# Performance work log

Measured on AMD Instinct MI355X. Metric: run time of the kernel, lower is better.

The kernel has to match this reference:

```python
import jax, jax.numpy as jnp
import numpy as np

B, S, D, H = 2, 2048, 2048, 16
HD = D // H  # head_dim = 128


def setup_inputs() -> dict:
    key = jax.random.key(0)
    ks = jax.random.split(key, 9)
    std = 0.02
    x = jax.random.normal(ks[0], (B, S, D), dtype=jnp.float32)
    Wq = jax.random.normal(ks[1], (D, D), dtype=jnp.float32) * std
    bq = jnp.zeros((D,), dtype=jnp.float32)
    Wk = jax.random.normal(ks[2], (D, D), dtype=jnp.float32) * std
    bk = jnp.zeros((D,), dtype=jnp.float32)
    Wv = jax.random.normal(ks[3], (D, D), dtype=jnp.float32) * std
    bv = jnp.zeros((D,), dtype=jnp.float32)
    Wo = jax.random.normal(ks[4], (D, D), dtype=jnp.float32) * std
    bo = jnp.zeros((D,), dtype=jnp.float32)
    return {"x": x, "Wq": Wq, "bq": bq, "Wk": Wk, "bk": bk,
            "Wv": Wv, "bv": bv, "Wo": Wo, "bo": bo}


def _rope_tables(seq_len, head_dim, base=10000.0):
    # inv_freq over even indices; freqs: [S, HD/2]
    inv_freq = 1.0 / (base ** (jnp.arange(0, head_dim, 2, dtype=jnp.float32) / head_dim))
    t = jnp.arange(seq_len, dtype=jnp.float32)
    freqs = jnp.einsum('i,j->ij', t, inv_freq)
    return jnp.cos(freqs), jnp.sin(freqs)  # each [S, HD/2]


def _rotate(x, cos, sin):
    # x: [B, H, S, HD]; cos/sin: [S, HD/2] broadcast over B,H
    x1, x2 = jnp.split(x, 2, axis=-1)
    return jnp.concatenate([x1 * cos - x2 * sin, x1 * sin + x2 * cos], axis=-1)


def reference(x, Wq, bq, Wk, bk, Wv, bv, Wo, bo):
    b, s, d = x.shape
    q = (jnp.einsum('bsd,df->bsf', x, Wq) + bq).reshape(b, s, H, HD).transpose(0, 2, 1, 3)
    k = (jnp.einsum('bsd,df->bsf', x, Wk) + bk).reshape(b, s, H, HD).transpose(0, 2, 1, 3)
    v = (jnp.einsum('bsd,df->bsf', x, Wv) + bv).reshape(b, s, H, HD).transpose(0, 2, 1, 3)
    cos, sin = _rope_tables(s, HD)
    qr = _rotate(q, cos, sin)
    kr = _rotate(k, cos, sin)
    scores = jnp.einsum('bhqd,bhkd->bhqk', qr, kr) / jnp.sqrt(jnp.float32(HD))
    probs = jax.nn.softmax(scores, axis=-1)
    out = jnp.einsum('bhqk,bhkd->bhqd', probs, v)
    out = out.transpose(0, 2, 1, 3).reshape(b, s, d)
    return jnp.einsum('bsd,df->bsf', out, Wo) + bo
```

## Files before the change

kernel.cpp:

```cpp
#include <hip/hip_runtime.h>

#define BB  2
#define SS  2048
#define DD  2048
#define HH  16
#define HDD 128
#define BSR 4096

using short8  = __attribute__((ext_vector_type(8))) short;
using floatx4 = __attribute__((ext_vector_type(4))) float;

__device__ __forceinline__ float bf2f(unsigned short u) {
  return __uint_as_float(((unsigned int)u) << 16);
}
__device__ __forceinline__ unsigned short f2bf(float f) {
  unsigned int u = __float_as_uint(f);
  u += 0x7fffu + ((u >> 16) & 1u);
  return (unsigned short)(u >> 16);
}
__device__ __forceinline__ unsigned int pk2bf(float a, float b) {
  unsigned int ua = __float_as_uint(a);
  ua += 0x7fffu + ((ua >> 16) & 1u);
  unsigned int ub = __float_as_uint(b);
  ub += 0x7fffu + ((ub >> 16) & 1u);
  return (ua >> 16) | (ub & 0xffff0000u);
}
__device__ __forceinline__ float fexp2(float x) {
#if __has_builtin(__builtin_amdgcn_exp2f)
  return __builtin_amdgcn_exp2f(x);
#else
  return __expf(x * 0.6931471805599453f);
#endif
}
__device__ __forceinline__ void gl_lds16(const void* g, void* l) {
  __builtin_amdgcn_global_load_lds(
      (__attribute__((address_space(1))) void*)g,
      (__attribute__((address_space(3))) void*)l, 16, 0, 0);
}

__global__ __launch_bounds__(256) void transpose_w(
    const float* __restrict__ Wq, const float* __restrict__ Wk,
    const float* __restrict__ Wv, const float* __restrict__ Wo,
    unsigned short* __restrict__ wqkvt, unsigned short* __restrict__ wot)
{
  __shared__ float tile[32][33];
  const float* W; unsigned short* Out;
  int z = blockIdx.z;
  if      (z == 0) { W = Wq; Out = wqkvt; }
  else if (z == 1) { W = Wk; Out = wqkvt + (size_t)DD * DD; }
  else if (z == 2) { W = Wv; Out = wqkvt + 2 * (size_t)DD * DD; }
  else             { W = Wo; Out = wot; }
  int tx = threadIdx.x, ty = threadIdx.y;
  int d0 = blockIdx.y * 32, f0 = blockIdx.x * 32;
#pragma unroll
  for (int i = 0; i < 4; i++)
    tile[ty + i * 8][tx] = W[(size_t)(d0 + ty + i * 8) * DD + f0 + tx];
  __syncthreads();
#pragma unroll
  for (int i = 0; i < 4; i++)
    Out[(size_t)(f0 + ty + i * 8) * DD + d0 + tx] = f2bf(tile[tx][ty + i * 8]);
}

__global__ __launch_bounds__(256) void conv_x(const float* __restrict__ x,
                                              unsigned short* __restrict__ xb)
{
  size_t i = ((size_t)blockIdx.x * 256 + threadIdx.x) * 4;
  float4 v = *(const float4*)(x + i);
  ushort4 o;
  o.x = f2bf(v.x); o.y = f2bf(v.y); o.z = f2bf(v.z); o.w = f2bf(v.w);
  *(ushort4*)(xb + i) = o;
}

__global__ __launch_bounds__(256) void rope_tab(float2* __restrict__ rtab) {
  int idx = blockIdx.x * 256 + threadIdx.x;
  int s = idx >> 6, c = idx & 63;
  float inv = powf(10000.f, -(float)c * (1.f / 64.f));
  float ang = (float)s * inv;
  float sn, cc;
  sincosf(ang, &sn, &cc);
  rtab[idx] = make_float2(cc, sn);
}

#define MFMA_QUAD(MB, NB, FB) \
  _Pragma("unroll") for (int m_ = 0; m_ < 4; m_++) \
  _Pragma("unroll") for (int n_ = 0; n_ < 2; n_++) \
  _Pragma("unroll") for (int kk_ = 0; kk_ < 2; kk_++) \
    acc[(MB)+m_][(NB)+n_] = __builtin_amdgcn_mfma_f32_16x16x32_bf16( \
        fa[m_][kk_], FB[n_][kk_], acc[(MB)+m_][(NB)+n_], 0, 0, 0);
#define BARX __builtin_amdgcn_s_barrier()

__global__ __launch_bounds__(512) void gemm_qkv(
    const unsigned short* __restrict__ A, const unsigned short* __restrict__ Bt,
    const float* __restrict__ bq, const float* __restrict__ bk,
    const float* __restrict__ bv, const float2* __restrict__ rtab,
    unsigned short* __restrict__ q_r, unsigned short* __restrict__ k_r,
    unsigned short* __restrict__ v_t)
{
  __shared__ unsigned short smem[65536];
  unsigned short* const AsP[2] = { smem,         smem + 32768 };
  unsigned short* const BsP[2] = { smem + 16384, smem + 49152 };
  const int K = DD;
  int t = threadIdx.x;
  int lane = t & 63, qd = lane >> 4, l16 = lane & 15;
  int w = t >> 6, wr = w >> 2, wc = w & 3;

  int bid = blockIdx.y * gridDim.x + blockIdx.x;
  int wg  = (bid & 7) * 48 + (bid >> 3);
  int n0 = (wg % 24) * 256;
  int m0 = (wg / 24) * 256;

  floatx4 zero4 = {0.f, 0.f, 0.f, 0.f};
  floatx4 acc[8][4];
#pragma unroll
  for (int i = 0; i < 8; i++)
#pragma unroll
    for (int j = 0; j < 4; j++) acc[i][j] = zero4;

  int srow = t >> 3;
  int schunk = ((t & 7) ^ (srow & 7)) * 8;
  const unsigned short* Ag = A  + (size_t)(m0 + srow) * K + schunk;
  const unsigned short* Bg = Bt + (size_t)(n0 + srow) * K + schunk;

  auto stA = [&](int bf, int kt, int half) {
#pragma unroll
    for (int q = 0; q < 2; q++) {
      int c = half * 2 + q;
      gl_lds16(Ag + (size_t)c * 64 * K + kt * 64, AsP[bf] + ((size_t)c * 512 + t) * 8);
    }
  };
  auto stB = [&](int bf, int kt, int half) {
#pragma unroll
    for (int q = 0; q < 2; q++) {
      int c = half * 2 + q;
      gl_lds16(Bg + (size_t)c * 64 * K + kt * 64, BsP[bf] + ((size_t)c * 512 + t) * 8);
    }
  };
  auto ldA = [&](int bf, int mf, int kk) -> short8 {
    int row = wr * 128 + mf * 16 + l16;
    return *(const short8*)&AsP[bf][row * 64 + (((kk * 4 + qd) ^ (l16 & 7)) * 8)];
  };
  auto ldB = [&](int bf, int nf, int kk) -> short8 {
    int row = wc * 64 + nf * 16 + l16;
    return *(const short8*)&BsP[bf][row * 64 + (((kk * 4 + qd) ^ (l16 & 7)) * 8)];
  };

  stA(0, 0, 0); stA(0, 0, 1); stB(0, 0, 0); stB(0, 0, 1);
  stA(1, 1, 0);
  asm volatile("s_waitcnt vmcnt(2)" ::: "memory");
  BARX;

  short8 fa[4][2], fbl[2][2], fbh[2][2];

#pragma unroll 1
  for (int i = 0; i < 16; i++) {
    const bool full = (i < 15);
    const int kt1 = 2 * i + 1, kt2 = 2 * i + 2, kt3 = 2 * i + 3;

#pragma unroll
    for (int m = 0; m < 4; m++) { fa[m][0] = ldA(0, m, 0); fa[m][1] = ldA(0, m, 1); }
#pragma unroll
    for (int n = 0; n < 2; n++) { fbl[n][0] = ldB(0, n, 0); fbl[n][1] = ldB(0, n, 1); }
    stA(1, kt1, 1);
    BARX;
    __builtin_amdgcn_s_setprio(1);
    MFMA_QUAD(0, 0, fbl);
    __builtin_amdgcn_s_setprio(0);
    BARX;
#pragma unroll
    for (int n = 0; n < 2; n++) { fbh[n][0] = ldB(0, 2 + n, 0); fbh[n][1] = ldB(0, 2 + n, 1); }
    stB(1, kt1, 0);
    BARX;
    __builtin_amdgcn_s_setprio(1);
    MFMA_QUAD(0, 2, fbh);
    __builtin_amdgcn_s_setprio(0);
    BARX;
#pragma unroll
    for (int m = 0; m < 4; m++) { fa[m][0] = ldA(0, 4 + m, 0); fa[m][1] = ldA(0, 4 + m, 1); }
    stB(1, kt1, 1);
    BARX;
    __builtin_amdgcn_s_setprio(1);
    MFMA_QUAD(4, 0, fbl);
    __builtin_amdgcn_s_setprio(0);
    BARX;
    if (full) stA(0, kt2, 0);
    BARX;
    __builtin_amdgcn_s_setprio(1);
    MFMA_QUAD(4, 2, fbh);
    __builtin_amdgcn_s_setprio(0);
    if (full) asm volatile("s_waitcnt vmcnt(2)" ::: "memory");
    else      asm volatile("s_waitcnt vmcnt(0)" ::: "memory");
    BARX;

#pragma unroll
    for (int m = 0; m < 4; m++) { fa[m][0] = ldA(1, m, 0); fa[m][1] = ldA(1, m, 1); }
#pragma unroll
    for (int n = 0; n < 2; n++) { fbl[n][0] = ldB(1, n, 0); fbl[n][1] = ldB(1, n, 1); }
    if (full) stA(0, kt2, 1);
    BARX;
    __builtin_amdgcn_s_setprio(1);
    MFMA_QUAD(0, 0, fbl);
    __builtin_amdgcn_s_setprio(0);
    BARX;
#pragma unroll
    for (int n = 0; n < 2; n++) { fbh[n][0] = ldB(1, 2 + n, 0); fbh[n][1] = ldB(1, 2 + n, 1); }
    if (full) stB(0, kt2, 0);
    BARX;
    __builtin_amdgcn_s_setprio(1);
    MFMA_QUAD(0, 2, fbh);
    __builtin_amdgcn_s_setprio(0);
    BARX;
#pragma unroll
    for (int m = 0; m < 4; m++) { fa[m][0] = ldA(1, 4 + m, 0); fa[m][1] = ldA(1, 4 + m, 1); }
    if (full) stB(0, kt2, 1);
    BARX;
    __builtin_amdgcn_s_setprio(1);
    MFMA_QUAD(4, 0, fbl);
    __builtin_amdgcn_s_setprio(0);
    BARX;
    if (full) stA(1, kt3, 0);
    BARX;
    __builtin_amdgcn_s_setprio(1);
    MFMA_QUAD(4, 2, fbh);
    __builtin_amdgcn_s_setprio(0);
    if (full) asm volatile("s_waitcnt vmcnt(2)" ::: "memory");
    else      asm volatile("s_waitcnt vmcnt(0)" ::: "memory");
    BARX;
  }

  __syncthreads();
  int plane = n0 >> 11;
  int h0 = (n0 >> 7) & 15;
  const float* bias = plane == 0 ? bq : (plane == 1 ? bk : bv);
  int bI = m0 >> 11, sbase = m0 & (SS - 1);
  const int CT = 258;
  unsigned short* Ct = smem;

#pragma unroll 1
  for (int half = 0; half < 2; half++) {
    if (wr == half) {
#pragma unroll
      for (int mf = 0; mf < 8; mf++)
#pragma unroll
        for (int nf = 0; nf < 4; nf++) {
          int rl = mf * 16 + qd * 4;
          int cl = wc * 64 + nf * 16 + l16;
          float bsv = bias[h0 * 128 + cl];
#pragma unroll
          for (int r = 0; r < 4; r++)
            Ct[(rl + r) * CT + cl] = f2bf(acc[mf][nf][r] + bsv);
        }
    }
    __syncthreads();
    if (plane < 2) {
      unsigned short* dst0 = (plane == 0 ? q_r : k_r) + (size_t)(bI * HH + h0) * SS * HDD;
      const float fac = (plane == 0) ? 0.12751744f : 1.0f;
#pragma unroll
      for (int it = 0; it < 16; it++) {
        int idx = it * 512 + t;
        int rl = idx >> 6;
        int u = idx & 63; int hh = u >> 5; int c2 = (u & 31) * 2;
        int s = sbase + half * 128 + rl;
        float4 cs = *(const float4*)&rtab[(size_t)s * 64 + c2];
        int cb = hh * 128 + c2;
        float a0 = bf2f(Ct[rl * CT + cb]);
        float a1 = bf2f(Ct[rl * CT + cb + 1]);
        float b0 = bf2f(Ct[rl * CT + cb + 64]);
        float b1 = bf2f(Ct[rl * CT + cb + 65]);
        unsigned int lo = pk2bf((a0 * cs.x - b0 * cs.y) * fac,
                                (a1 * cs.z - b1 * cs.w) * fac);
        unsigned int hi = pk2bf((a0 * cs.y + b0 * cs.x) * fac,
                                (a1 * cs.w + b1 * cs.z) * fac);
        unsigned short* dst = dst0 + (size_t)hh * SS * HDD;
        size_t rowb = (size_t)s * HDD;
        *(unsigned int*)&dst[rowb + c2]      = lo;
        *(unsigned int*)&dst[rowb + c2 + 64] = hi;
      }
    } else {
      unsigned short* dst0 = v_t + (size_t)(bI * HH + h0) * HDD * SS;
#pragma unroll
      for (int it = 0; it < 32; it++) {
        int idx = it * 512 + t;
        int hdg = idx >> 6;
        int sp = (idx & 63) * 2;
        unsigned short v0 = Ct[sp * CT + hdg];
        unsigned short v1 = Ct[(sp + 1) * CT + hdg];
        int hh = hdg >> 7, hd = hdg & 127;
        int y = sp & 63;
        int kap = ((y >> 5) & 1) * 32 + ((y >> 2) & 3) * 8 + ((y >> 4) & 1) * 4 + (y & 3);
        int sg = sbase + half * 128 + (sp & ~63) + kap;
        unsigned short* dst = dst0 + (size_t)hh * HDD * SS;
        *(unsigned int*)&dst[(size_t)hd * SS + sg] = ((unsigned int)v1 << 16) | v0;
      }
    }
    if (half == 0) __syncthreads();
  }
}

template <bool OUTF32>
__global__ __launch_bounds__(256) void gemm_bt(
    const unsigned short* __restrict__ A, const unsigned short* __restrict__ Bt,
    const float* __restrict__ bias, void* __restrict__ Cout,
    int M, int N, int K)
{
  __shared__ unsigned short As[128 * 64];
  __shared__ unsigned short Bs[128 * 64];
  int t = threadIdx.x;
  int m0 = blockIdx.y * 128, n0 = blockIdx.x * 128;
  int w = t >> 6, lane = t & 63, qd = lane >> 4, l16 = lane & 15;
  int wm = (w >> 1) * 64, wn = (w & 1) * 64;
  floatx4 zero4 = {0.f, 0.f, 0.f, 0.f};
  floatx4 acc[4][4];
#pragma unroll
  for (int i = 0; i < 4; i++)
#pragma unroll
    for (int j = 0; j < 4; j++) acc[i][j] = zero4;

  int gchunk = (t & 7) ^ ((t >> 3) & 7);
  const unsigned short* Ab = A  + (size_t)(m0 + (t >> 3)) * K + gchunk * 8;
  const unsigned short* Bb = Bt + (size_t)(n0 + (t >> 3)) * K + gchunk * 8;
  size_t qK = (size_t)32 * K;

  for (int k0 = 0; k0 < K; k0 += 64) {
    __syncthreads();
#pragma unroll
    for (int c = 0; c < 4; c++) {
      gl_lds16(Ab + c * qK + k0, &As[(c * 256 + t) * 8]);
      gl_lds16(Bb + c * qK + k0, &Bs[(c * 256 + t) * 8]);
    }
    __syncthreads();
#pragma unroll
    for (int ks = 0; ks < 2; ks++) {
      int ch = ((ks * 4 + qd) ^ (l16 & 7)) * 8;
      short8 af[4], bfr[4];
#pragma unroll
      for (int i = 0; i < 4; i++)
        af[i] = *(const short8*)&As[(wm + i * 16 + l16) * 64 + ch];
#pragma unroll
      for (int j = 0; j < 4; j++)
        bfr[j] = *(const short8*)&Bs[(wn + j * 16 + l16) * 64 + ch];
#pragma unroll
      for (int i = 0; i < 4; i++)
#pragma unroll
        for (int j = 0; j < 4; j++)
          acc[i][j] = __builtin_amdgcn_mfma_f32_16x16x32_bf16(af[i], bfr[j], acc[i][j], 0, 0, 0);
    }
  }

#pragma unroll
  for (int i = 0; i < 4; i++)
#pragma unroll
    for (int j = 0; j < 4; j++) {
      int row = m0 + wm + i * 16 + qd * 4;
      int col = n0 + wn + j * 16 + l16;
      float bsv = bias ? bias[col] : 0.f;
#pragma unroll
      for (int r = 0; r < 4; r++) {
        float v = acc[i][j][r] + bsv;
        if (OUTF32) ((float*)Cout)[(size_t)(row + r) * N + col] = v;
        else ((unsigned short*)Cout)[(size_t)(row + r) * N + col] = f2bf(v);
      }
    }
}

__global__ __launch_bounds__(256, 2) void attn_kernel(
    const unsigned short* __restrict__ q_r, const unsigned short* __restrict__ k_r,
    const unsigned short* __restrict__ v_t, unsigned short* __restrict__ aout)
{
  __shared__ unsigned short Ks[2][64 * 128];
  __shared__ unsigned short Vs[2][128 * 64];
  int t = threadIdx.x, w = t >> 6, lane = t & 63, qd = lane >> 4, l16 = lane & 15;
  int L = blockIdx.y * gridDim.x + blockIdx.x;
  int jj = L >> 3;
  int bh = (L & 7) * 4 + (jj >> 4);
  int q0 = (jj & 15) * 128;
  const unsigned short* qb = q_r + (size_t)bh * SS * HDD;
  const unsigned short* kb = k_r + (size_t)bh * SS * HDD;
  const unsigned short* vb = v_t + (size_t)bh * HDD * SS;

  short8 aq[2][4];
#pragma unroll
  for (int mi = 0; mi < 2; mi++)
#pragma unroll
    for (int ks = 0; ks < 4; ks++)
      aq[mi][ks] = *(const short8*)
          &qb[(size_t)(q0 + w * 32 + mi * 16 + l16) * HDD + ks * 32 + qd * 8];

  float m_i[2], l_i[2];
  floatx4 zero4 = {0.f, 0.f, 0.f, 0.f};
  floatx4 o[2][8];
#pragma unroll
  for (int mi = 0; mi < 2; mi++) { m_i[mi] = -1e30f; l_i[mi] = 0.f; }
#pragma unroll
  for (int mi = 0; mi < 2; mi++)
#pragma unroll
    for (int n = 0; n < 8; n++) o[mi][n] = zero4;

  auto stage = [&](int nb, int kt) {
#pragma unroll
    for (int c = 0; c < 4; c++) {
      int flat = c * 256 + t;
      int r = flat >> 4, cc = flat & 15;
      gl_lds16(kb + (size_t)(kt + r) * HDD + (cc ^ (r & 15)) * 8, &Ks[nb][flat * 8]);
    }
#pragma unroll
    for (int c = 0; c < 4; c++) {
      int flat = c * 256 + t;
      int r = flat >> 3, cc = flat & 7;
      gl_lds16(vb + (size_t)r * SS + kt + (cc ^ (r & 7)) * 8, &Vs[nb][flat * 8]);
    }
  };

  stage(0, 0);
  int buf = 0;

  for (int kt = 0; kt < SS; kt += 64) {
    __syncthreads();
    if (kt + 64 < SS) stage(buf ^ 1, kt + 64);

    floatx4 sc[2][4];
#pragma unroll
    for (int mi = 0; mi < 2; mi++)
#pragma unroll
      for (int j = 0; j < 4; j++) sc[mi][j] = zero4;
#pragma unroll
    for (int j = 0; j < 4; j++) {
      int krow = j * 16 + l16;
#pragma unroll
      for (int ks = 0; ks < 4; ks++) {
        int chunk = ks * 4 + qd;
        short8 kf = *(const short8*)&Ks[buf][krow * 128 + ((chunk ^ (krow & 15)) * 8)];
        sc[0][j] = __builtin_amdgcn_mfma_f32_16x16x32_bf16(kf, aq[0][ks], sc[0][j], 0, 0, 0);
        sc[1][j] = __builtin_amdgcn_mfma_f32_16x16x32_bf16(kf, aq[1][ks], sc[1][j], 0, 0, 0);
      }
    }

    float rmax[2];
#pragma unroll
    for (int mi = 0; mi < 2; mi++) {
      float m = sc[mi][0][0];
#pragma unroll
      for (int j = 0; j < 4; j++)
#pragma unroll
        for (int r = 0; r < 4; r++) m = fmaxf(m, sc[mi][j][r]);
      m = fmaxf(m, __shfl_xor(m, 16, 64));
      m = fmaxf(m, __shfl_xor(m, 32, 64));
      rmax[mi] = m;
    }

    bool up = (rmax[0] > m_i[0]) || (rmax[1] > m_i[1]);
    if (__ballot(up) != 0ull) {
#pragma unroll
      for (int mi = 0; mi < 2; mi++) {
        float mn = fmaxf(m_i[mi], rmax[mi]);
        float a = fexp2(m_i[mi] - mn);
        m_i[mi] = mn;
        l_i[mi] *= a;
#pragma unroll
        for (int n = 0; n < 8; n++)
#pragma unroll
          for (int r = 0; r < 4; r++) o[mi][n][r] *= a;
      }
    }

    unsigned int pr[2][4][2];
#pragma unroll
    for (int mi = 0; mi < 2; mi++) {
      float s0 = 0.f;
#pragma unroll
      for (int j = 0; j < 4; j++) {
        float p0 = fexp2(sc[mi][j][0] - m_i[mi]);
        float p1 = fexp2(sc[mi][j][1] - m_i[mi]);
        float p2 = fexp2(sc[mi][j][2] - m_i[mi]);
        float p3 = fexp2(sc[mi][j][3] - m_i[mi]);
        s0 += (p0 + p1) + (p2 + p3);
        pr[mi][j][0] = pk2bf(p0, p1);
        pr[mi][j][1] = pk2bf(p2, p3);
      }
      s0 += __shfl_xor(s0, 16, 64);
      s0 += __shfl_xor(s0, 32, 64);
      l_i[mi] += s0;
    }

#pragma unroll
    for (int n = 0; n < 8; n++) {
      int vrow = n * 16 + l16;
#pragma unroll
      for (int ks = 0; ks < 2; ks++) {
        int chunk = ks * 4 + qd;
        short8 av = *(const short8*)&Vs[buf][vrow * 64 + ((chunk ^ (vrow & 7)) * 8)];
        union { unsigned int u[4]; short8 v; } bp0, bp1;
        bp0.u[0] = pr[0][2 * ks][0];     bp0.u[1] = pr[0][2 * ks][1];
        bp0.u[2] = pr[0][2 * ks + 1][0]; bp0.u[3] = pr[0][2 * ks + 1][1];
        bp1.u[0] = pr[1][2 * ks][0];     bp1.u[1] = pr[1][2 * ks][1];
        bp1.u[2] = pr[1][2 * ks + 1][0]; bp1.u[3] = pr[1][2 * ks + 1][1];
        o[0][n] = __builtin_amdgcn_mfma_f32_16x16x32_bf16(av, bp0.v, o[0][n], 0, 0, 0);
        o[1][n] = __builtin_amdgcn_mfma_f32_16x16x32_bf16(av, bp1.v, o[1][n], 0, 0, 0);
      }
    }
    buf ^= 1;
  }

  int b = bh >> 4, h = bh & 15;
#pragma unroll
  for (int mi = 0; mi < 2; mi++) {
    int qrow = q0 + w * 32 + mi * 16 + l16;
    float inv_l = 1.f / l_i[mi];
    size_t base = ((size_t)(b * SS + qrow)) * DD + h * HDD;
#pragma unroll
    for (int n = 0; n < 8; n++) {
      uint2 pkd;
      pkd.x = pk2bf(o[mi][n][0] * inv_l, o[mi][n][1] * inv_l);
      pkd.y = pk2bf(o[mi][n][2] * inv_l, o[mi][n][3] * inv_l);
      *(uint2*)&aout[base + n * 16 + qd * 4] = pkd;
    }
  }
}

extern "C" void kernel_launch(void* const* d_in, const int* in_sizes, int n_in,
                              void* d_out, int out_size, void* d_ws, size_t ws_size,
                              hipStream_t stream) {
  const float* x  = (const float*)d_in[0];
  const float* Wq = (const float*)d_in[1];
  const float* bq = (const float*)d_in[2];
  const float* Wk = (const float*)d_in[3];
  const float* bk = (const float*)d_in[4];
  const float* Wv = (const float*)d_in[5];
  const float* bv = (const float*)d_in[6];
  const float* Wo = (const float*)d_in[7];
  const float* bo = (const float*)d_in[8];
  float* out = (float*)d_out;

  char* ws = (char*)d_ws;
  unsigned short* xb      = (unsigned short*)(ws + 0);
  unsigned short* wqkvt   = (unsigned short*)(ws + 16777216);
  unsigned short* wot     = (unsigned short*)(ws + 41943040);
  float2*         rtab    = (float2*)(ws + 50331648);
  unsigned short* q_r     = (unsigned short*)(ws + 100663296);
  unsigned short* k_r     = (unsigned short*)(ws + 117440512);
  unsigned short* v_t     = (unsigned short*)(ws + 134217728);
  unsigned short* attn_o  = xb;

  transpose_w<<<dim3(DD / 32, DD / 32, 4), dim3(32, 8), 0, stream>>>(
      Wq, Wk, Wv, Wo, wqkvt, wot);
  conv_x<<<dim3((BSR * DD) / 1024), dim3(256), 0, stream>>>(x, xb);
  rope_tab<<<dim3((SS * 64) / 256), dim3(256), 0, stream>>>(rtab);
  gemm_qkv<<<dim3(3 * DD / 256, BSR / 256), dim3(512), 0, stream>>>(
      xb, wqkvt, bq, bk, bv, rtab, q_r, k_r, v_t);
  attn_kernel<<<dim3(SS / 128, BB * HH), dim3(256), 0, stream>>>(
      q_r, k_r, v_t, attn_o);
  gemm_bt<true><<<dim3(DD / 128, BSR / 128), dim3(256), 0, stream>>>(
      attn_o, wot, bo, out, BSR, DD, DD);
}
```

Baseline: 411.7 us.

## Shrink QKV GEMM tile to 128x256 and rework k-loop pipeline

The fused QKV GEMM block tile shrinks from 256x256 to 128x256, which doubles the grid to 768 blocks and halves the accumulator registers and A-tile LDS. The k-loop is rewritten as a KTILE macro that prefetches the tile two steps ahead into the same buffer, with vmcnt(6) waits. The aim is more blocks for the 256 CUs and higher occupancy from fewer registers and less LDS. The cost is lower arithmetic intensity per block, so B (weight) tiles are reloaded twice as often. The epilogue becomes a single pass because the 128-row tile fits the transpose buffer.

```diff
diff --git a/kernel.cpp b/kernel.cpp
--- a/kernel.cpp
+++ b/kernel.cpp
@@ -81,13 +81,37 @@
   rtab[idx] = make_float2(cc, sn);
 }
 
-#define MFMA_QUAD(MB, NB, FB) \
-  _Pragma("unroll") for (int m_ = 0; m_ < 4; m_++) \
+#define MFMA_Q(MB, NB, FA, FB) \
+  _Pragma("unroll") for (int m_ = 0; m_ < 2; m_++) \
   _Pragma("unroll") for (int n_ = 0; n_ < 2; n_++) \
   _Pragma("unroll") for (int kk_ = 0; kk_ < 2; kk_++) \
     acc[(MB)+m_][(NB)+n_] = __builtin_amdgcn_mfma_f32_16x16x32_bf16( \
-        fa[m_][kk_], FB[n_][kk_], acc[(MB)+m_][(NB)+n_], 0, 0, 0);
+        (FA)[m_][kk_], (FB)[n_][kk_], acc[(MB)+m_][(NB)+n_], 0, 0, 0);
 #define BARX __builtin_amdgcn_s_barrier()
+
+#define KTILE(BF, KT, FULL) do {                                               \
+  _Pragma("unroll")                                                            \
+  for (int m = 0; m < 2; m++) { fa[m][0] = ldA(BF, m, 0); fa[m][1] = ldA(BF, m, 1); } \
+  _Pragma("unroll")                                                            \
+  for (int n = 0; n < 2; n++) { fbl[n][0] = ldB(BF, n, 0); fbl[n][1] = ldB(BF, n, 1); } \
+  BARX; __builtin_amdgcn_s_setprio(1); MFMA_Q(0, 0, fa, fbl);                  \
+  __builtin_amdgcn_s_setprio(0); BARX;                                         \
+  _Pragma("unroll")                                                            \
+  for (int n = 0; n < 2; n++) { fbh[n][0] = ldB(BF, 2 + n, 0); fbh[n][1] = ldB(BF, 2 + n, 1); } \
+  BARX; __builtin_amdgcn_s_setprio(1); MFMA_Q(0, 2, fa, fbh);                  \
+  __builtin_amdgcn_s_setprio(0); BARX;                                         \
+  _Pragma("unroll")                                                            \
+  for (int m = 0; m < 2; m++) { fa2[m][0] = ldA(BF, 2 + m, 0); fa2[m][1] = ldA(BF, 2 + m, 1); } \
+  if (FULL) stB(BF, (KT) + 2, 0);                                              \
+  BARX; __builtin_amdgcn_s_setprio(1); MFMA_Q(2, 0, fa2, fbl);                 \
+  __builtin_amdgcn_s_setprio(0); BARX;                                         \
+  if (FULL) { stB(BF, (KT) + 2, 1); stA(BF, (KT) + 2); }                       \
+  BARX; __builtin_amdgcn_s_setprio(1); MFMA_Q(2, 2, fa2, fbh);                 \
+  __builtin_amdgcn_s_setprio(0);                                               \
+  if (FULL) asm volatile("s_waitcnt vmcnt(6)" ::: "memory");                   \
+  else      asm volatile("s_waitcnt vmcnt(0)" ::: "memory");                   \
+  BARX;                                                                        \
+} while (0)
 
 __global__ __launch_bounds__(512) void gemm_qkv(
     const unsigned short* __restrict__ A, const unsigned short* __restrict__ Bt,
@@ -96,23 +120,23 @@
     unsigned short* __restrict__ q_r, unsigned short* __restrict__ k_r,
     unsigned short* __restrict__ v_t)
 {
-  __shared__ unsigned short smem[65536];
-  unsigned short* const AsP[2] = { smem,         smem + 32768 };
-  unsigned short* const BsP[2] = { smem + 16384, smem + 49152 };
+  __shared__ unsigned short smem[49152];
+  unsigned short* const AsP[2] = { smem,          smem + 24576 };
+  unsigned short* const BsP[2] = { smem + 8192,   smem + 32768 };
   const int K = DD;
   int t = threadIdx.x;
   int lane = t & 63, qd = lane >> 4, l16 = lane & 15;
   int w = t >> 6, wr = w >> 2, wc = w & 3;
 
-  int bid = blockIdx.y * gridDim.x + blockIdx.x;
-  int wg  = (bid & 7) * 48 + (bid >> 3);
-  int n0 = (wg % 24) * 256;
-  int m0 = (wg / 24) * 256;
+  int bid = blockIdx.x;
+  int wg  = (bid & 7) * 96 + (bid >> 3);
+  int n0 = (wg / 32) * 256;
+  int m0 = (wg % 32) * 128;
 
   floatx4 zero4 = {0.f, 0.f, 0.f, 0.f};
-  floatx4 acc[8][4];
-#pragma unroll
-  for (int i = 0; i < 8; i++)
+  floatx4 acc[4][4];
+#pragma unroll
+  for (int i = 0; i < 4; i++)
 #pragma unroll
     for (int j = 0; j < 4; j++) acc[i][j] = zero4;
 
@@ -121,12 +145,10 @@
   const unsigned short* Ag = A  + (size_t)(m0 + srow) * K + schunk;
   const unsigned short* Bg = Bt + (size_t)(n0 + srow) * K + schunk;
 
-  auto stA = [&](int bf, int kt, int half) {
-#pragma unroll
-    for (int q = 0; q < 2; q++) {
-      int c = half * 2 + q;
+  auto stA = [&](int bf, int kt) {
+#pragma unroll
+    for (int c = 0; c < 2; c++)
       gl_lds16(Ag + (size_t)c * 64 * K + kt * 64, AsP[bf] + ((size_t)c * 512 + t) * 8);
-    }
   };
   auto stB = [&](int bf, int kt, int half) {
 #pragma unroll
@@ -136,7 +158,7 @@
     }
   };
   auto ldA = [&](int bf, int mf, int kk) -> short8 {
-    int row = wr * 128 + mf * 16 + l16;
+    int row = wr * 64 + mf * 16 + l16;
     return *(const short8*)&AsP[bf][row * 64 + (((kk * 4 + qd) ^ (l16 & 7)) * 8)];
   };
   auto ldB = [&](int bf, int nf, int kk) -> short8 {
@@ -144,87 +166,18 @@
     return *(const short8*)&BsP[bf][row * 64 + (((kk * 4 + qd) ^ (l16 & 7)) * 8)];
   };
 
-  stA(0, 0, 0); stA(0, 0, 1); stB(0, 0, 0); stB(0, 0, 1);
-  stA(1, 1, 0);
-  asm volatile("s_waitcnt vmcnt(2)" ::: "memory");
+  stA(0, 0); stB(0, 0, 0); stB(0, 0, 1);
+  stA(1, 1); stB(1, 1, 0); stB(1, 1, 1);
+  asm volatile("s_waitcnt vmcnt(6)" ::: "memory");
   BARX;
 
-  short8 fa[4][2], fbl[2][2], fbh[2][2];
+  short8 fa[2][2], fa2[2][2], fbl[2][2], fbh[2][2];
 
 #pragma unroll 1
   for (int i = 0; i < 16; i++) {
     const bool full = (i < 15);
-    const int kt1 = 2 * i + 1, kt2 = 2 * i + 2, kt3 = 2 * i + 3;
-
-#pragma unroll
-    for (int m = 0; m < 4; m++) { fa[m][0] = ldA(0, m, 0); fa[m][1] = ldA(0, m, 1); }
-#pragma unroll
-    for (int n = 0; n < 2; n++) { fbl[n][0] = ldB(0, n, 0); fbl[n][1] = ldB(0, n, 1); }
-    stA(1, kt1, 1);
-    BARX;
-    __builtin_amdgcn_s_setprio(1);
-    MFMA_QUAD(0, 0, fbl);
-    __builtin_amdgcn_s_setprio(0);
-    BARX;
-#pragma unroll
-    for (int n = 0; n < 2; n++) { fbh[n][0] = ldB(0, 2 + n, 0); fbh[n][1] = ldB(0, 2 + n, 1); }
-    stB(1, kt1, 0);
-    BARX;
-    __builtin_amdgcn_s_setprio(1);
-    MFMA_QUAD(0, 2, fbh);
-    __builtin_amdgcn_s_setprio(0);
-    BARX;
-#pragma unroll
-    for (int m = 0; m < 4; m++) { fa[m][0] = ldA(0, 4 + m, 0); fa[m][1] = ldA(0, 4 + m, 1); }
-    stB(1, kt1, 1);
-    BARX;
-    __builtin_amdgcn_s_setprio(1);
-    MFMA_QUAD(4, 0, fbl);
-    __builtin_amdgcn_s_setprio(0);
-    BARX;
-    if (full) stA(0, kt2, 0);
-    BARX;
-    __builtin_amdgcn_s_setprio(1);
-    MFMA_QUAD(4, 2, fbh);
-    __builtin_amdgcn_s_setprio(0);
-    if (full) asm volatile("s_waitcnt vmcnt(2)" ::: "memory");
-    else      asm volatile("s_waitcnt vmcnt(0)" ::: "memory");
-    BARX;
-
-#pragma unroll
-    for (int m = 0; m < 4; m++) { fa[m][0] = ldA(1, m, 0); fa[m][1] = ldA(1, m, 1); }
-#pragma unroll
-    for (int n = 0; n < 2; n++) { fbl[n][0] = ldB(1, n, 0); fbl[n][1] = ldB(1, n, 1); }
-    if (full) stA(0, kt2, 1);
-    BARX;
-    __builtin_amdgcn_s_setprio(1);
-    MFMA_QUAD(0, 0, fbl);
-    __builtin_amdgcn_s_setprio(0);
-    BARX;
-#pragma unroll
-    for (int n = 0; n < 2; n++) { fbh[n][0] = ldB(1, 2 + n, 0); fbh[n][1] = ldB(1, 2 + n, 1); }
-    if (full) stB(0, kt2, 0);
-    BARX;
-    __builtin_amdgcn_s_setprio(1);
-    MFMA_QUAD(0, 2, fbh);
-    __builtin_amdgcn_s_setprio(0);
-    BARX;
-#pragma unroll
-    for (int m = 0; m < 4; m++) { fa[m][0] = ldA(1, 4 + m, 0); fa[m][1] = ldA(1, 4 + m, 1); }
-    if (full) stB(0, kt2, 1);
-    BARX;
-    __builtin_amdgcn_s_setprio(1);
-    MFMA_QUAD(4, 0, fbl);
-    __builtin_amdgcn_s_setprio(0);
-    BARX;
-    if (full) stA(1, kt3, 0);
-    BARX;
-    __builtin_amdgcn_s_setprio(1);
-    MFMA_QUAD(4, 2, fbh);
-    __builtin_amdgcn_s_setprio(0);
-    if (full) asm volatile("s_waitcnt vmcnt(2)" ::: "memory");
-    else      asm volatile("s_waitcnt vmcnt(0)" ::: "memory");
-    BARX;
+    KTILE(0, 2 * i,     full);
+    KTILE(1, 2 * i + 1, full);
   }
 
   __syncthreads();
@@ -235,64 +188,59 @@
   const int CT = 258;
   unsigned short* Ct = smem;
 
-#pragma unroll 1
-  for (int half = 0; half < 2; half++) {
-    if (wr == half) {
-#pragma unroll
-      for (int mf = 0; mf < 8; mf++)
-#pragma unroll
-        for (int nf = 0; nf < 4; nf++) {
-          int rl = mf * 16 + qd * 4;
-          int cl = wc * 64 + nf * 16 + l16;
-          float bsv = bias[h0 * 128 + cl];
-#pragma unroll
-          for (int r = 0; r < 4; r++)
-            Ct[(rl + r) * CT + cl] = f2bf(acc[mf][nf][r] + bsv);
-        }
-    }
-    __syncthreads();
-    if (plane < 2) {
-      unsigned short* dst0 = (plane == 0 ? q_r : k_r) + (size_t)(bI * HH + h0) * SS * HDD;
-      const float fac = (plane == 0) ? 0.12751744f : 1.0f;
-#pragma unroll
-      for (int it = 0; it < 16; it++) {
-        int idx = it * 512 + t;
-        int rl = idx >> 6;
-        int u = idx & 63; int hh = u >> 5; int c2 = (u & 31) * 2;
-        int s = sbase + half * 128 + rl;
-        float4 cs = *(const float4*)&rtab[(size_t)s * 64 + c2];
-        int cb = hh * 128 + c2;
-        float a0 = bf2f(Ct[rl * CT + cb]);
-        float a1 = bf2f(Ct[rl * CT + cb + 1]);
-        float b0 = bf2f(Ct[rl * CT + cb + 64]);
-        float b1 = bf2f(Ct[rl * CT + cb + 65]);
-        unsigned int lo = pk2bf((a0 * cs.x - b0 * cs.y) * fac,
-                                (a1 * cs.z - b1 * cs.w) * fac);
-        unsigned int hi = pk2bf((a0 * cs.y + b0 * cs.x) * fac,
-                                (a1 * cs.w + b1 * cs.z) * fac);
-        unsigned short* dst = dst0 + (size_t)hh * SS * HDD;
-        size_t rowb = (size_t)s * HDD;
-        *(unsigned int*)&dst[rowb + c2]      = lo;
-        *(unsigned int*)&dst[rowb + c2 + 64] = hi;
-      }
-    } else {
-      unsigned short* dst0 = v_t + (size_t)(bI * HH + h0) * HDD * SS;
-#pragma unroll
-      for (int it = 0; it < 32; it++) {
-        int idx = it * 512 + t;
-        int hdg = idx >> 6;
-        int sp = (idx & 63) * 2;
-        unsigned short v0 = Ct[sp * CT + hdg];
-        unsigned short v1 = Ct[(sp + 1) * CT + hdg];
-        int hh = hdg >> 7, hd = hdg & 127;
-        int y = sp & 63;
-        int kap = ((y >> 5) & 1) * 32 + ((y >> 2) & 3) * 8 + ((y >> 4) & 1) * 4 + (y & 3);
-        int sg = sbase + half * 128 + (sp & ~63) + kap;
-        unsigned short* dst = dst0 + (size_t)hh * HDD * SS;
-        *(unsigned int*)&dst[(size_t)hd * SS + sg] = ((unsigned int)v1 << 16) | v0;
-      }
-    }
-    if (half == 0) __syncthreads();
+#pragma unroll
+  for (int mf = 0; mf < 4; mf++)
+#pragma unroll
+    for (int nf = 0; nf < 4; nf++) {
+      int rl = wr * 64 + mf * 16 + qd * 4;
+      int cl = wc * 64 + nf * 16 + l16;
+      float bsv = bias[h0 * 128 + cl];
+#pragma unroll
+      for (int r = 0; r < 4; r++)
+        Ct[(rl + r) * CT + cl] = f2bf(acc[mf][nf][r] + bsv);
+    }
+  __syncthreads();
+
+  if (plane < 2) {
+    unsigned short* dst0 = (plane == 0 ? q_r : k_r) + (size_t)(bI * HH + h0) * SS * HDD;
+    const float fac = (plane == 0) ? 0.12751744f : 1.0f;
+#pragma unroll
+    for (int it = 0; it < 16; it++) {
+      int idx = it * 512 + t;
+      int rl = idx >> 6;
+      int u = idx & 63; int hh = u >> 5; int c2 = (u & 31) * 2;
+      int s = sbase + rl;
+      float4 cs = *(const float4*)&rtab[(size_t)s * 64 + c2];
+      int cb = hh * 128 + c2;
+      float a0 = bf2f(Ct[rl * CT + cb]);
+      float a1 = bf2f(Ct[rl * CT + cb + 1]);
+      float b0 = bf2f(Ct[rl * CT + cb + 64]);
+      float b1 = bf2f(Ct[rl * CT + cb + 65]);
+      unsigned int lo = pk2bf((a0 * cs.x - b0 * cs.y) * fac,
+                              (a1 * cs.z - b1 * cs.w) * fac);
+      unsigned int hi = pk2bf((a0 * cs.y + b0 * cs.x) * fac,
+                              (a1 * cs.w + b1 * cs.z) * fac);
+      unsigned short* dst = dst0 + (size_t)hh * SS * HDD;
+      size_t rowb = (size_t)s * HDD;
+      *(unsigned int*)&dst[rowb + c2]      = lo;
+      *(unsigned int*)&dst[rowb + c2 + 64] = hi;
+    }
+  } else {
+    unsigned short* dst0 = v_t + (size_t)(bI * HH + h0) * HDD * SS;
+#pragma unroll
+    for (int it = 0; it < 32; it++) {
+      int idx = it * 512 + t;
+      int hdg = idx >> 6;
+      int sp = (idx & 63) * 2;
+      unsigned short v0 = Ct[sp * CT + hdg];
+      unsigned short v1 = Ct[(sp + 1) * CT + hdg];
+      int hh = hdg >> 7, hd = hdg & 127;
+      int y = sp & 63;
+      int kap = ((y >> 5) & 1) * 32 + ((y >> 2) & 3) * 8 + ((y >> 4) & 1) * 4 + (y & 3);
+      int sg = sbase + (sp & ~63) + kap;
+      unsigned short* dst = dst0 + (size_t)hh * HDD * SS;
+      *(unsigned int*)&dst[(size_t)hd * SS + sg] = ((unsigned int)v1 << 16) | v0;
+    }
   }
 }
 
@@ -544,7 +492,7 @@
       Wq, Wk, Wv, Wo, wqkvt, wot);
   conv_x<<<dim3((BSR * DD) / 1024), dim3(256), 0, stream>>>(x, xb);
   rope_tab<<<dim3((SS * 64) / 256), dim3(256), 0, stream>>>(rtab);
-  gemm_qkv<<<dim3(3 * DD / 256, BSR / 256), dim3(512), 0, stream>>>(
+  gemm_qkv<<<dim3(768), dim3(512), 0, stream>>>(
       xb, wqkvt, bq, bk, bv, rtab, q_r, k_r, v_t);
   attn_kernel<<<dim3(SS / 128, BB * HH), dim3(256), 0, stream>>>(
       q_r, k_r, v_t, attn_o);
```

Result: faster. 400.3 us (-2.8%).
